# Optimization experiments

Measured on AMD Instinct MI355X. Metric: run time of the kernel, lower is better.

Reference implementation:

```python
import jax, jax.numpy as jnp
import numpy as np

B, T, C, H = 2, 2048, 1024, 16
D = C // H
THETA = 10000.0


def setup_inputs() -> dict:
    key = jax.random.key(0)
    k1, k2, k3 = jax.random.split(key, 3)
    x = jax.random.normal(k1, (B, T, C), dtype=jnp.float32)
    tok_mask = jnp.ones((B, T), dtype=bool)
    # torch Linear weights stored transposed: y = x @ W.T; we store [in, out]
    W_qkv = jax.random.normal(k2, (C, 3 * C), dtype=jnp.float32) / np.sqrt(C)
    W_o = jax.random.normal(k3, (C, C), dtype=jnp.float32) / np.sqrt(C)
    return {"x": x, "tok_mask": tok_mask, "W_qkv": W_qkv, "W_o": W_o}


def _rope_tables(t_len):
    # NOTE: source uses exponents arange(1, D+1, 2)/D and positions starting at 1
    exps = jnp.arange(1, D + 1, 2, dtype=jnp.float32)[: D // 2] / D
    w = 1.0 / (THETA ** exps)                      # [D/2]
    t = jnp.arange(1, t_len + 1, dtype=jnp.float32)  # [T]
    ang = t[:, None] * w[None, :]                  # [T, D/2]
    return jnp.sin(ang), jnp.cos(ang)


def _rope(x, sin, cos):
    # x: [B, H, T, D]; rotate interleaved pairs
    x1 = x[..., ::2]
    x2 = x[..., 1::2]
    r1 = x1 * cos - x2 * sin
    r2 = x1 * sin + x2 * cos
    return jnp.stack((r1, r2), axis=-1).reshape(x.shape)


def reference(x, tok_mask, W_qkv, W_o):
    b, t, c = x.shape
    qkv = x @ W_qkv                                   # [B,T,3C]
    q, k, v = jnp.split(qkv, 3, axis=-1)
    def heads(z):
        return z.reshape(b, t, H, D).transpose(0, 2, 1, 3)  # [B,H,T,D]
    q, k, v = heads(q), heads(k), heads(v)
    sin, cos = _rope_tables(t)
    q = _rope(q, sin, cos)
    k = _rope(k, sin, cos)
    scores = jnp.einsum('bhqd,bhkd->bhqk', q, k) / jnp.sqrt(jnp.float32(D))
    # mask[b,i,j] = tok_mask[b,i] & tok_mask[b,j] & causal
    mask = tok_mask[:, None, :, None] & tok_mask[:, None, None, :]  # [B,1,T,T]
    causal = jnp.tril(jnp.ones((t, t), dtype=bool))
    mask = mask & causal[None, None, :, :]
    scores = jnp.where(mask, scores, jnp.float32(-1e9))
    att = jax.nn.softmax(scores, axis=-1)             # dropout p=0 (eval)
    y = jnp.einsum('bhqk,bhkd->bhqd', att, v)
    y = y.transpose(0, 2, 1, 3).reshape(b, t, c)
    return y @ W_o
```

## Files before the change

kernel.cpp:

```cpp
#include <hip/hip_runtime.h>
#include <hip/hip_bf16.h>

typedef __bf16 bf16x8 __attribute__((ext_vector_type(8)));
typedef short s16x4 __attribute__((ext_vector_type(4)));
typedef float floatx4 __attribute__((ext_vector_type(4)));
typedef __hip_bfloat16 bf16;

#define T_SEQ 2048
#define NH 16
#define HD 64
#define CDIM 1024

__device__ __forceinline__ void gload16(const bf16* g, bf16* ldsbase) {
  __builtin_amdgcn_global_load_lds((const __attribute__((address_space(1))) void*)g,
                                   (__attribute__((address_space(3))) void*)ldsbase, 16, 0, 0);
}

__global__ __launch_bounds__(256) void prep_kernel(const float* __restrict__ x,
                                                   const float* __restrict__ Wqkv,
                                                   const float* __restrict__ Wo,
                                                   bf16* __restrict__ Xb,
                                                   bf16* __restrict__ WqkvT,
                                                   bf16* __restrict__ WoT,
                                                   float2* __restrict__ tab) {
  __shared__ float tile[32][33];
  const int bid = blockIdx.x, tid = threadIdx.x;
  if (bid < 4096) {
    int i = bid * 256 + tid;
    const float4 v = ((const float4*)x)[i];
    union { bf16 h[4]; uint2 u; } pk;
    pk.h[0] = __float2bfloat16(v.x);
    pk.h[1] = __float2bfloat16(v.y);
    pk.h[2] = __float2bfloat16(v.z);
    pk.h[3] = __float2bfloat16(v.w);
    ((uint2*)Xb)[i] = pk.u;
  } else if (bid < 8192) {
    const float* in;
    bf16* out;
    int bx, by, R, Cc;
    if (bid < 7168) {
      int t = bid - 4096;
      in = Wqkv; out = WqkvT; R = 1024; Cc = 3072;
      bx = (t % 96) * 32; by = (t / 96) * 32;
    } else {
      int t = bid - 7168;
      in = Wo; out = WoT; R = 1024; Cc = 1024;
      bx = (t & 31) * 32; by = (t >> 5) * 32;
    }
    const int tx = tid & 31, ty = tid >> 5;
#pragma unroll
    for (int i = 0; i < 32; i += 8)
      tile[ty + i][tx] = in[(size_t)(by + ty + i) * Cc + bx + tx];
    __syncthreads();
#pragma unroll
    for (int i = 0; i < 32; i += 8)
      out[(size_t)(bx + ty + i) * R + by + tx] = __float2bfloat16(tile[tx][ty + i]);
  } else {
    int idx = (bid - 8192) * 256 + tid;
    int t = idx >> 5, j = idx & 31;
    float w = exp2f(-13.287712379549449f * (float)(2 * j + 1) * (1.0f / 64.0f));
    float ang = (float)(t + 1) * w;
    tab[idx] = make_float2(cosf(ang), sinf(ang));
  }
}

template <int MODE>
__global__ __launch_bounds__(256) void gemm_bt(
    const bf16* __restrict__ A, const bf16* __restrict__ BT, float* __restrict__ CoutF,
    const float2* __restrict__ tab, bf16* __restrict__ Qr, bf16* __restrict__ Kr,
    bf16* __restrict__ Vt, int M, int N, int K) {
  constexpr int LDK = 32;
  __shared__ __align__(16) bf16 As[128 * LDK];
  __shared__ __align__(16) bf16 Bs[128 * LDK];
  const int tid = threadIdx.x, lane = tid & 63, wave = tid >> 6;
  const int quad = lane >> 4, c16 = lane & 15;
  const int tile_m = blockIdx.y * 128, tile_n = blockIdx.x * 128;
  const int wm = (wave >> 1) * 64, wn = (wave & 1) * 64;
  const int r0 = tid >> 2, cp4 = tid & 3;
  const int csw = (cp4 ^ ((r0 >> 1) & 3)) * 8;
  const int swr = (quad ^ ((c16 >> 1) & 3)) * 8;
  bf16* ldsA0 = &As[wave * 512];
  bf16* ldsA1 = &As[2048 + wave * 512];
  bf16* ldsB0 = &Bs[wave * 512];
  bf16* ldsB1 = &Bs[2048 + wave * 512];
  floatx4 acc[4][4] = {};
  for (int k0 = 0; k0 < K; k0 += 32) {
    __syncthreads();
    gload16(&A[(size_t)(tile_m + r0) * K + k0 + csw], ldsA0);
    gload16(&A[(size_t)(tile_m + r0 + 64) * K + k0 + csw], ldsA1);
    gload16(&BT[(size_t)(tile_n + r0) * K + k0 + csw], ldsB0);
    gload16(&BT[(size_t)(tile_n + r0 + 64) * K + k0 + csw], ldsB1);
    __syncthreads();
    bf16x8 af[4], bfr[4];
#pragma unroll
    for (int i = 0; i < 4; i++)
      af[i] = *(const bf16x8*)&As[(wm + i * 16 + c16) * LDK + swr];
#pragma unroll
    for (int i = 0; i < 4; i++)
      bfr[i] = *(const bf16x8*)&Bs[(wn + i * 16 + c16) * LDK + swr];
#pragma unroll
    for (int mi = 0; mi < 4; mi++)
#pragma unroll
      for (int ni = 0; ni < 4; ni++)
        acc[mi][ni] = __builtin_amdgcn_mfma_f32_16x16x32_bf16(af[mi], bfr[ni], acc[mi][ni], 0, 0, 0);
  }
  if (MODE == 0) {
#pragma unroll
    for (int mi = 0; mi < 4; mi++) {
      int row0 = tile_m + wm + mi * 16 + quad * 4;
#pragma unroll
      for (int ni = 0; ni < 4; ni++) {
        int col = tile_n + wn + ni * 16 + c16;
#pragma unroll
        for (int r = 0; r < 4; r++)
          CoutF[(size_t)(row0 + r) * N + col] = acc[mi][ni][r];
      }
    }
  } else {
#pragma unroll
    for (int ni = 0; ni < 4; ni++) {
      int colg = tile_n + wn + ni * 16 + c16;
      int seg = colg >> 10;
      int cc = colg & 1023;
      int h = cc >> 6, d = cc & 63, j = d >> 1;
#pragma unroll
      for (int mi = 0; mi < 4; mi++) {
        int row0 = tile_m + wm + mi * 16 + quad * 4;
#pragma unroll
        for (int r = 0; r < 4; r++) {
          int rowg = row0 + r;
          int b = rowg >> 11, t = rowg & 2047;
          float val = acc[mi][ni][r];
          float partner = __shfl_xor(val, 1, 64);
          size_t bh = (size_t)(b * NH + h);
          if (seg == 2) {
            Vt[(bh * HD + d) * T_SEQ + t] = __float2bfloat16(val);
          } else {
            float2 sc = tab[t * 32 + j];
            float outv = ((d & 1) == 0) ? (val * sc.x - partner * sc.y)
                                        : (val * sc.x + partner * sc.y);
            bf16* dst = (seg == 0) ? Qr : Kr;
            dst[(bh * T_SEQ + t) * HD + d] = __float2bfloat16(outv);
          }
        }
      }
    }
  }
}

__global__ __launch_bounds__(256) void attn_kernel(const bf16* __restrict__ Qr,
                                                   const bf16* __restrict__ Kr,
                                                   const bf16* __restrict__ Vt,
                                                   bf16* __restrict__ Y) {
  constexpr int DPAD = 68;
  __shared__ __align__(16) bf16 Ks[2][64 * DPAD];
  __shared__ __align__(16) bf16 Vs[2][64 * DPAD];
  __shared__ __align__(16) bf16 Ps[4][16 * DPAD];
  const int qtile = 31 - (blockIdx.x >> 5), bh = blockIdx.x & 31;
  const int b = bh >> 4, h = bh & 15;
  const int tid = threadIdx.x, lane = tid & 63, wave = tid >> 6;
  const int quad = lane >> 4, c16 = lane & 15;
  const size_t hoff = (size_t)bh * T_SEQ * HD;
  const int row0 = tid >> 3, cp = tid & 7;
  const int qbase = qtile * 64;
  const int qg = qbase + wave * 16 + c16;
  bf16x8 qf0 = *(const bf16x8*)&Qr[hoff + (size_t)qg * HD + quad * 8];
  bf16x8 qf1 = *(const bf16x8*)&Qr[hoff + (size_t)qg * HD + 32 + quad * 8];
  floatx4 o_acc[4] = {};
  float m_run = -1e30f, l_run = 0.f;
  bf16x8 kreg0 = *(const bf16x8*)&Kr[hoff + (size_t)row0 * HD + cp * 8];
  bf16x8 kreg1 = *(const bf16x8*)&Kr[hoff + (size_t)(row0 + 32) * HD + cp * 8];
  bf16x8 vreg0 = *(const bf16x8*)&Vt[hoff + (size_t)row0 * T_SEQ + cp * 8];
  bf16x8 vreg1 = *(const bf16x8*)&Vt[hoff + (size_t)(row0 + 32) * T_SEQ + cp * 8];
  *(bf16x8*)&Ks[0][row0 * DPAD + cp * 8] = kreg0;
  *(bf16x8*)&Ks[0][(row0 + 32) * DPAD + cp * 8] = kreg1;
  *(bf16x8*)&Vs[0][row0 * DPAD + cp * 8] = vreg0;
  *(bf16x8*)&Vs[0][(row0 + 32) * DPAD + cp * 8] = vreg1;
  __syncthreads();
  for (int kt = 0; kt <= qtile; ++kt) {
    const int kbase = kt * 64;
    const int cur = kt & 1;
    if (kt < qtile) {
      const int nb = kbase + 64;
      kreg0 = *(const bf16x8*)&Kr[hoff + (size_t)(nb + row0) * HD + cp * 8];
      kreg1 = *(const bf16x8*)&Kr[hoff + (size_t)(nb + row0 + 32) * HD + cp * 8];
      vreg0 = *(const bf16x8*)&Vt[hoff + (size_t)row0 * T_SEQ + nb + cp * 8];
      vreg1 = *(const bf16x8*)&Vt[hoff + (size_t)(row0 + 32) * T_SEQ + nb + cp * 8];
    }
    floatx4 s[4];
#pragma unroll
    for (int nt = 0; nt < 4; nt++) {
      bf16x8 kf0 = *(const bf16x8*)&Ks[cur][(nt * 16 + c16) * DPAD + quad * 8];
      bf16x8 kf1 = *(const bf16x8*)&Ks[cur][(nt * 16 + c16) * DPAD + 32 + quad * 8];
      floatx4 z = {0.f, 0.f, 0.f, 0.f};
      z = __builtin_amdgcn_mfma_f32_16x16x32_bf16(kf0, qf0, z, 0, 0, 0);
      z = __builtin_amdgcn_mfma_f32_16x16x32_bf16(kf1, qf1, z, 0, 0, 0);
      s[nt] = z;
    }
    const bool diag = (kt == qtile);
    float mloc = -1e30f;
#pragma unroll
    for (int nt = 0; nt < 4; nt++)
#pragma unroll
      for (int r = 0; r < 4; r++) {
        float v = s[nt][r] * 0.125f;
        if (diag) {
          int kg = kbase + nt * 16 + quad * 4 + r;
          v = (kg <= qg) ? v : -1e30f;
        }
        s[nt][r] = v;
        mloc = fmaxf(mloc, v);
      }
    mloc = fmaxf(mloc, __shfl_xor(mloc, 16, 64));
    mloc = fmaxf(mloc, __shfl_xor(mloc, 32, 64));
    float mn = fmaxf(m_run, mloc);
    float alpha = __expf(m_run - mn);
    m_run = mn;
    float lloc = 0.f;
    union { bf16 h[4]; s16x4 sv; } ph[4];
#pragma unroll
    for (int nt = 0; nt < 4; nt++)
#pragma unroll
      for (int r = 0; r < 4; r++) {
        float pp = __expf(s[nt][r] - mn);
        lloc += pp;
        ph[nt].h[r] = __float2bfloat16(pp);
      }
    lloc += __shfl_xor(lloc, 16, 64);
    lloc += __shfl_xor(lloc, 32, 64);
    l_run = l_run * alpha + lloc;
#pragma unroll
    for (int nt = 0; nt < 4; nt++)
      *(s16x4*)&Ps[wave][c16 * DPAD + nt * 16 + quad * 4] = ph[nt].sv;
    float a_bc[4];
#pragma unroll
    for (int r = 0; r < 4; r++) a_bc[r] = __shfl(alpha, quad * 4 + r, 16);
#pragma unroll
    for (int dt = 0; dt < 4; dt++)
#pragma unroll
      for (int r = 0; r < 4; r++) o_acc[dt][r] *= a_bc[r];
    bf16x8 pf0 = *(const bf16x8*)&Ps[wave][c16 * DPAD + quad * 8];
    bf16x8 pf1 = *(const bf16x8*)&Ps[wave][c16 * DPAD + 32 + quad * 8];
#pragma unroll
    for (int dt = 0; dt < 4; dt++) {
      bf16x8 vf0 = *(const bf16x8*)&Vs[cur][(dt * 16 + c16) * DPAD + quad * 8];
      bf16x8 vf1 = *(const bf16x8*)&Vs[cur][(dt * 16 + c16) * DPAD + 32 + quad * 8];
      o_acc[dt] = __builtin_amdgcn_mfma_f32_16x16x32_bf16(pf0, vf0, o_acc[dt], 0, 0, 0);
      o_acc[dt] = __builtin_amdgcn_mfma_f32_16x16x32_bf16(pf1, vf1, o_acc[dt], 0, 0, 0);
    }
    if (kt < qtile) {
      const int nxt = cur ^ 1;
      *(bf16x8*)&Ks[nxt][row0 * DPAD + cp * 8] = kreg0;
      *(bf16x8*)&Ks[nxt][(row0 + 32) * DPAD + cp * 8] = kreg1;
      *(bf16x8*)&Vs[nxt][row0 * DPAD + cp * 8] = vreg0;
      *(bf16x8*)&Vs[nxt][(row0 + 32) * DPAD + cp * 8] = vreg1;
    }
    __syncthreads();
  }
  float linv = 1.0f / l_run;
  float l_bc[4];
#pragma unroll
  for (int r = 0; r < 4; r++) l_bc[r] = __shfl(linv, quad * 4 + r, 16);
#pragma unroll
  for (int dt = 0; dt < 4; dt++)
#pragma unroll
    for (int r = 0; r < 4; r++) {
      int t = qbase + wave * 16 + quad * 4 + r;
      Y[((size_t)(b * T_SEQ + t)) * CDIM + h * HD + dt * 16 + c16] =
          __float2bfloat16(o_acc[dt][r] * l_bc[r]);
    }
}

extern "C" void kernel_launch(void* const* d_in, const int* in_sizes, int n_in,
                              void* d_out, int out_size, void* d_ws, size_t ws_size,
                              hipStream_t stream) {
  const float* x    = (const float*)d_in[0];
  const float* Wqkv = (const float*)d_in[2];
  const float* Wo   = (const float*)d_in[3];
  float* out = (float*)d_out;

  bf16* ws    = (bf16*)d_ws;
  bf16* Xb    = ws;
  bf16* WqkvT = Xb + 4194304;
  bf16* WoT   = WqkvT + 3072 * 1024;
  bf16* Qr    = WoT + 1024 * 1024;
  bf16* Kr    = Qr + 4194304;
  bf16* Vt    = Kr + 4194304;
  bf16* Y     = Vt + 4194304;
  float2* tab = (float2*)(Y + 4194304);

  prep_kernel<<<dim3(8448), 256, 0, stream>>>(x, Wqkv, Wo, Xb, WqkvT, WoT, tab);
  gemm_bt<1><<<dim3(3072 / 128, 4096 / 128), 256, 0, stream>>>(
      Xb, WqkvT, nullptr, tab, Qr, Kr, Vt, 4096, 3072, 1024);
  attn_kernel<<<dim3(1024), 256, 0, stream>>>(Qr, Kr, Vt, Y);
  gemm_bt<0><<<dim3(1024 / 128, 4096 / 128), 256, 0, stream>>>(
      Y, WoT, out, nullptr, nullptr, nullptr, nullptr, 4096, 1024, 1024);
}
```

Before: 208.3 us.

## Double-buffer GEMM LDS tiles and fold softmax scale into Q projection

```diff
diff --git a/kernel.cpp b/kernel.cpp
--- a/kernel.cpp
+++ b/kernel.cpp
@@ -70,8 +70,8 @@
     const float2* __restrict__ tab, bf16* __restrict__ Qr, bf16* __restrict__ Kr,
     bf16* __restrict__ Vt, int M, int N, int K) {
   constexpr int LDK = 32;
-  __shared__ __align__(16) bf16 As[128 * LDK];
-  __shared__ __align__(16) bf16 Bs[128 * LDK];
+  __shared__ __align__(16) bf16 As[2][128 * LDK];
+  __shared__ __align__(16) bf16 Bs[2][128 * LDK];
   const int tid = threadIdx.x, lane = tid & 63, wave = tid >> 6;
   const int quad = lane >> 4, c16 = lane & 15;
   const int tile_m = blockIdx.y * 128, tile_n = blockIdx.x * 128;
@@ -79,25 +79,31 @@
   const int r0 = tid >> 2, cp4 = tid & 3;
   const int csw = (cp4 ^ ((r0 >> 1) & 3)) * 8;
   const int swr = (quad ^ ((c16 >> 1) & 3)) * 8;
-  bf16* ldsA0 = &As[wave * 512];
-  bf16* ldsA1 = &As[2048 + wave * 512];
-  bf16* ldsB0 = &Bs[wave * 512];
-  bf16* ldsB1 = &Bs[2048 + wave * 512];
   floatx4 acc[4][4] = {};
-  for (int k0 = 0; k0 < K; k0 += 32) {
+  const bf16* aRow0 = &A[(size_t)(tile_m + r0) * K + csw];
+  const bf16* aRow1 = &A[(size_t)(tile_m + r0 + 64) * K + csw];
+  const bf16* bRow0 = &BT[(size_t)(tile_n + r0) * K + csw];
+  const bf16* bRow1 = &BT[(size_t)(tile_n + r0 + 64) * K + csw];
+  gload16(aRow0, &As[0][wave * 512]);
+  gload16(aRow1, &As[0][2048 + wave * 512]);
+  gload16(bRow0, &Bs[0][wave * 512]);
+  gload16(bRow1, &Bs[0][2048 + wave * 512]);
+  int buf = 0;
+  for (int k0 = 0; k0 < K; k0 += 32, buf ^= 1) {
     __syncthreads();
-    gload16(&A[(size_t)(tile_m + r0) * K + k0 + csw], ldsA0);
-    gload16(&A[(size_t)(tile_m + r0 + 64) * K + k0 + csw], ldsA1);
-    gload16(&BT[(size_t)(tile_n + r0) * K + k0 + csw], ldsB0);
-    gload16(&BT[(size_t)(tile_n + r0 + 64) * K + k0 + csw], ldsB1);
-    __syncthreads();
+    if (k0 + 32 < K) {
+      const int kn = k0 + 32, nb = buf ^ 1;
+      gload16(aRow0 + kn, &As[nb][wave * 512]);
+      gload16(aRow1 + kn, &As[nb][2048 + wave * 512]);
+      gload16(bRow0 + kn, &Bs[nb][wave * 512]);
+      gload16(bRow1 + kn, &Bs[nb][2048 + wave * 512]);
+    }
     bf16x8 af[4], bfr[4];
 #pragma unroll
-    for (int i = 0; i < 4; i++)
-      af[i] = *(const bf16x8*)&As[(wm + i * 16 + c16) * LDK + swr];
-#pragma unroll
-    for (int i = 0; i < 4; i++)
-      bfr[i] = *(const bf16x8*)&Bs[(wn + i * 16 + c16) * LDK + swr];
+    for (int i = 0; i < 4; i++) {
+      af[i] = *(const bf16x8*)&As[buf][(wm + i * 16 + c16) * LDK + swr];
+      bfr[i] = *(const bf16x8*)&Bs[buf][(wn + i * 16 + c16) * LDK + swr];
+    }
 #pragma unroll
     for (int mi = 0; mi < 4; mi++)
 #pragma unroll
@@ -139,6 +145,7 @@
             float2 sc = tab[t * 32 + j];
             float outv = ((d & 1) == 0) ? (val * sc.x - partner * sc.y)
                                         : (val * sc.x + partner * sc.y);
+            if (seg == 0) outv *= 0.125f;
             bf16* dst = (seg == 0) ? Qr : Kr;
             dst[(bh * T_SEQ + t) * HD + d] = __float2bfloat16(outv);
           }
@@ -197,20 +204,23 @@
       z = __builtin_amdgcn_mfma_f32_16x16x32_bf16(kf1, qf1, z, 0, 0, 0);
       s[nt] = z;
     }
-    const bool diag = (kt == qtile);
     float mloc = -1e30f;
-#pragma unroll
-    for (int nt = 0; nt < 4; nt++)
-#pragma unroll
-      for (int r = 0; r < 4; r++) {
-        float v = s[nt][r] * 0.125f;
-        if (diag) {
+    if (kt == qtile) {
+#pragma unroll
+      for (int nt = 0; nt < 4; nt++)
+#pragma unroll
+        for (int r = 0; r < 4; r++) {
           int kg = kbase + nt * 16 + quad * 4 + r;
-          v = (kg <= qg) ? v : -1e30f;
+          float v = (kg <= qg) ? s[nt][r] : -1e30f;
+          s[nt][r] = v;
+          mloc = fmaxf(mloc, v);
         }
-        s[nt][r] = v;
-        mloc = fmaxf(mloc, v);
-      }
+    } else {
+#pragma unroll
+      for (int nt = 0; nt < 4; nt++)
+#pragma unroll
+        for (int r = 0; r < 4; r++) mloc = fmaxf(mloc, s[nt][r]);
+    }
     mloc = fmaxf(mloc, __shfl_xor(mloc, 16, 64));
     mloc = fmaxf(mloc, __shfl_xor(mloc, 32, 64));
     float mn = fmaxf(m_run, mloc);
```

New measurement: 201.5 us. 1.03x faster.
